# Optimization experiments

Measured on AMD Instinct MI355X. Metric: run time of the kernel, lower is better.

Reference implementation:

```python
import jax, jax.numpy as jnp
import numpy as np

N = 50000      # nodes
E = 400000     # edges
NODE_IN = 16
EDGE_IN = 8
H = 4          # heads (layer 1)
C = 64         # hidden_dim
HC = H * C     # 256


def setup_inputs() -> dict:
    key = jax.random.key(0)
    ks = iter(jax.random.split(key, 48))
    def rn(shape, s=0.05):
        return jax.random.normal(next(ks), shape, jnp.float32) * s
    x = jax.random.normal(next(ks), (N, NODE_IN), jnp.float32)
    edge_index = jax.random.randint(next(ks), (2, E), 0, N)
    edge_attr = jax.random.normal(next(ks), (E, EDGE_IN), jnp.float32)
    params = dict(
        # conv1: GATv2Conv(node_in -> hidden, heads=4, concat=True, edge_dim=edge_in)
        Wl1=rn((NODE_IN, HC)), bl1=jnp.zeros((HC,), jnp.float32),
        Wr1=rn((NODE_IN, HC)), br1=jnp.zeros((HC,), jnp.float32),
        We1=rn((EDGE_IN, HC)), att1=rn((H, C)), bias1=jnp.zeros((HC,), jnp.float32),
        # conv2: GATv2Conv(hidden*heads -> hidden, heads=1, concat=False)
        Wl2=rn((HC, C)), bl2=jnp.zeros((C,), jnp.float32),
        Wr2=rn((HC, C)), br2=jnp.zeros((C,), jnp.float32),
        We2=rn((EDGE_IN, C)), att2=rn((1, C)), bias2=jnp.zeros((C,), jnp.float32),
        # batchnorms (eval mode: running stats)
        bn1_g=jnp.ones((HC,), jnp.float32), bn1_b=jnp.zeros((HC,), jnp.float32),
        bn1_m=rn((HC,), 0.01), bn1_v=jnp.ones((HC,), jnp.float32),
        bn2_g=jnp.ones((C,), jnp.float32), bn2_b=jnp.zeros((C,), jnp.float32),
        bn2_m=rn((C,), 0.01), bn2_v=jnp.ones((C,), jnp.float32),
        # residual projection
        Wres=rn((NODE_IN, HC)),
        Wm1=rn((2 * C + EDGE_IN, C)), bm1=jnp.zeros((C,), jnp.float32),
        Wm2=rn((C, C // 2)), bm2=jnp.zeros((C // 2,), jnp.float32),
        Wm3=rn((C // 2, 1)), bm3=jnp.zeros((1,), jnp.float32),
    )
    return dict(x=x, edge_index=edge_index, edge_attr=edge_attr, **params)


def _gatv2(x, src, dst, e_attr, Wl, bl, Wr, br, We, att, bias, heads, out_ch, concat):
    """GATv2Conv message passing (PyG semantics, self-loops already in src/dst)."""
    n = x.shape[0]
    xl = (x @ Wl + bl).reshape(n, heads, out_ch)   # source transform
    xr = (x @ Wr + br).reshape(n, heads, out_ch)   # target transform
    ee = (e_attr @ We).reshape(-1, heads, out_ch)  # edge transform
    # per-edge attention logits: leaky_relu(x_i + x_j + e) . att
    m = jax.nn.leaky_relu(xl[src] + xr[dst] + ee, 0.2)        # [Etot, H, C]
    alpha = jnp.einsum('ehc,hc->eh', m, att)                  # [Etot, H]
    # segment softmax over destination nodes (every node has a self-loop)
    amax = jax.ops.segment_max(alpha, dst, num_segments=n)    # [N, H]
    expa = jnp.exp(alpha - amax[dst])
    denom = jax.ops.segment_sum(expa, dst, num_segments=n)    # [N, H]
    a = expa / (denom[dst] + 1e-16)
    out = jax.ops.segment_sum(xl[src] * a[:, :, None], dst, num_segments=n)  # [N, H, C]
    out = out.reshape(n, heads * out_ch) if concat else out.mean(axis=1)
    return out + bias


def _bn(h, g, b, m, v):
    return (h - m) * jax.lax.rsqrt(v + 1e-5) * g + b


def _forward(x, edge_attr, Wl1, bl1, Wr1, br1, We1, att1, bias1,
             Wl2, bl2, Wr2, br2, We2, att2, bias2,
             bn1_g, bn1_b, bn1_m, bn1_v, bn2_g, bn2_b, bn2_m, bn2_v,
             Wres, Wm1, bm1, Wm2, bm2, Wm3, bm3, edge_index):
    row, col = edge_index[0], edge_index[1]
    # add self-loops with fill_value='mean' for edge_attr (GATv2Conv default)
    loop = jnp.arange(N)
    src = jnp.concatenate([row, loop])
    dst = jnp.concatenate([col, loop])
    ea_mean = edge_attr.mean(axis=0, keepdims=True)
    ea_full = jnp.concatenate([edge_attr, jnp.broadcast_to(ea_mean, (N, EDGE_IN))], axis=0)
    h = _gatv2(x, src, dst, ea_full, Wl1, bl1, Wr1, br1, We1, att1, bias1, H, C, True)
    h = _bn(h, bn1_g, bn1_b, bn1_m, bn1_v)
    h = jax.nn.elu(h + x @ Wres)                 # residual; dropout is a no-op in eval
    h = _gatv2(h, src, dst, ea_full, Wl2, bl2, Wr2, br2, We2, att2, bias2, 1, C, False)
    h = _bn(h, bn2_g, bn2_b, bn2_m, bn2_v)
    h = jax.nn.elu(h)
    # edge head: gather endpoint embeddings + edge_attr -> MLP -> sigmoid
    er = jnp.concatenate([h[row], h[col], edge_attr], axis=-1)   # [E, 2C+edge_in]
    z = jax.nn.gelu(er @ Wm1 + bm1, approximate=False)
    z = jax.nn.gelu(z @ Wm2 + bm2, approximate=False)
    return jax.nn.sigmoid(z @ Wm3 + bm3)[:, 0]                    # [E]


def reference(x, edge_index, edge_attr, Wl1, bl1, Wr1, br1, We1, att1, bias1,
              Wl2, bl2, Wr2, br2, We2, att2, bias2,
              bn1_g, bn1_b, bn1_m, bn1_v, bn2_g, bn2_b, bn2_m, bn2_v,
              Wres, Wm1, bm1, Wm2, bm2, Wm3, bm3):
    return _forward(x, edge_attr, Wl1, bl1, Wr1, br1, We1, att1, bias1,
                    Wl2, bl2, Wr2, br2, We2, att2, bias2,
                    bn1_g, bn1_b, bn1_m, bn1_v, bn2_g, bn2_b, bn2_m, bn2_v,
                    Wres, Wm1, bm1, Wm2, bm2, Wm3, bm3, edge_index)
```

## Files before the change

kernel.cpp:

```cpp
#include <hip/hip_runtime.h>
#include <hip/hip_bf16.h>
#include <hip/hip_fp16.h>
#include <math.h>

#define NN 50000
#define EE 400000
#define ETOT (NN + EE)

__device__ __forceinline__ float gelu_f(float x) {
    return 0.5f * x * (1.f + erff(x * 0.7071067811865476f));
}
__device__ __forceinline__ float elu_f(float x) {
    return x > 0.f ? x : expm1f(x);
}
__device__ __forceinline__ float4 half8_lo_hi(uint4 raw, float4* hi) {
    __half2 h0 = *(__half2*)&raw.x, h1 = *(__half2*)&raw.y;
    __half2 h2 = *(__half2*)&raw.z, h3 = *(__half2*)&raw.w;
    float2 f0 = __half22float2(h0), f1 = __half22float2(h1);
    float2 f2 = __half22float2(h2), f3 = __half22float2(h3);
    *hi = make_float4(f2.x, f2.y, f3.x, f3.y);
    return make_float4(f0.x, f0.y, f1.x, f1.y);
}

__global__ __launch_bounds__(256) void k_ea_reduce(const float* __restrict__ ea,
                                                   float* __restrict__ ea_sum, int E) {
    float s[8];
#pragma unroll
    for (int i = 0; i < 8; i++) s[i] = 0.f;
    for (int e = blockIdx.x * blockDim.x + threadIdx.x; e < E; e += gridDim.x * blockDim.x) {
        const float4* p = (const float4*)(ea + (size_t)e * 8);
        float4 a = p[0], b = p[1];
        s[0] += a.x; s[1] += a.y; s[2] += a.z; s[3] += a.w;
        s[4] += b.x; s[5] += b.y; s[6] += b.z; s[7] += b.w;
    }
#pragma unroll
    for (int o = 32; o; o >>= 1)
#pragma unroll
        for (int i = 0; i < 8; i++) s[i] += __shfl_xor(s[i], o, 64);
    __shared__ float sh[4][8];
    int lane = threadIdx.x & 63, w = threadIdx.x >> 6;
    if (lane == 0)
#pragma unroll
        for (int i = 0; i < 8; i++) sh[w][i] = s[i];
    __syncthreads();
    if (threadIdx.x < 8) {
        float v = sh[0][threadIdx.x] + sh[1][threadIdx.x] + sh[2][threadIdx.x] + sh[3][threadIdx.x];
        atomicAdd(ea_sum + threadIdx.x, v);
    }
}

__global__ __launch_bounds__(256) void k_count(const int* __restrict__ ei, int* __restrict__ counts,
                                               int E, int N) {
    int e = blockIdx.x * blockDim.x + threadIdx.x;
    if (e >= E + N) return;
    int d = (e < E) ? ei[E + e] : (e - E);
    atomicAdd(counts + d, 1);
}

__global__ __launch_bounds__(1024) void k_scan(const int* __restrict__ counts, int* __restrict__ off,
                                               int* __restrict__ cursor, int N) {
    __shared__ int buf[1024];
    int t = threadIdx.x;
    int carry = 0;
    if (t == 0) off[0] = 0;
    for (int base = 0; base < N; base += 1024) {
        int i = base + t;
        int v = (i < N) ? counts[i] : 0;
        buf[t] = v;
        __syncthreads();
        for (int o = 1; o < 1024; o <<= 1) {
            int add = (t >= o) ? buf[t - o] : 0;
            __syncthreads();
            buf[t] += add;
            __syncthreads();
        }
        int incl = buf[t] + carry;
        if (i < N) { off[i + 1] = incl; cursor[i] = incl - v; }
        int tot = buf[1023];
        __syncthreads();
        carry += tot;
    }
}

__global__ __launch_bounds__(256) void k_scatter(const int* __restrict__ ei, int* __restrict__ cursor,
                                                 int* __restrict__ csr_src, int* __restrict__ csr_eid,
                                                 int E, int N) {
    int e = blockIdx.x * blockDim.x + threadIdx.x;
    if (e >= E + N) return;
    int s, d;
    if (e < E) { s = ei[e]; d = ei[E + e]; }
    else { s = d = e - E; }
    int pos = atomicAdd(cursor + d, 1);
    csr_src[pos] = s;
    csr_eid[pos] = e;
}

__global__ __launch_bounds__(256) void k_ntrans1(const float* __restrict__ x,
                                                 const float* __restrict__ Wl, const float* __restrict__ bl,
                                                 const float* __restrict__ Wr, const float* __restrict__ br,
                                                 __half* __restrict__ xl1h, float* __restrict__ xr1, int N) {
    __shared__ float swl[16 * 256];
    __shared__ float swr[16 * 256];
    __shared__ float sx[32 * 16];
    int t = threadIdx.x;
#pragma unroll
    for (int k = 0; k < 16; k++) { swl[k * 256 + t] = Wl[k * 256 + t]; swr[k * 256 + t] = Wr[k * 256 + t]; }
    int n0 = blockIdx.x * 32;
    for (int i = t; i < 32 * 16; i += 256) {
        int n = n0 + (i >> 4);
        sx[i] = (n < N) ? x[(size_t)n * 16 + (i & 15)] : 0.f;
    }
    __syncthreads();
    float bL = bl[t], bR = br[t];
    for (int ni = 0; ni < 32; ni++) {
        int n = n0 + ni;
        if (n >= N) break;
        float al = bL, ar = bR;
#pragma unroll
        for (int k = 0; k < 16; k++) {
            float xv = sx[ni * 16 + k];
            al += xv * swl[k * 256 + t];
            ar += xv * swr[k * 256 + t];
        }
        xl1h[(size_t)n * 256 + t] = __float2half(al);
        xr1[(size_t)n * 256 + t] = ar;
    }
}

__global__ __launch_bounds__(256) void k_fagg1(const __half* __restrict__ xl1h, const float* __restrict__ xr1,
                                               const int* __restrict__ off, const int* __restrict__ csr_src,
                                               const int* __restrict__ csr_eid,
                                               const float* __restrict__ ea, const float* __restrict__ ea_sum,
                                               const float* __restrict__ We1, const float* __restrict__ att1,
                                               const float* __restrict__ bias1,
                                               const float* __restrict__ x, const float* __restrict__ Wres,
                                               const float* __restrict__ g, const float* __restrict__ bb_,
                                               const float* __restrict__ mm_, const float* __restrict__ vv_,
                                               float* __restrict__ h1,
                                               int E, int N) {
    int t = threadIdx.x;
    int lane = t & 63, w = t >> 6;
    int node = blockIdx.x * 4 + w;
    if (node >= N) return;
    int c4 = lane * 4;
    float4 we[8];
#pragma unroll
    for (int k = 0; k < 8; k++) we[k] = *(const float4*)(We1 + k * 256 + c4);
    float4 xr4 = *(const float4*)(xr1 + (size_t)node * 256 + c4);
    float4 at4 = *(const float4*)(att1 + c4);
    float invE = 1.f / (float)E;
    float4 eam0, eam1;
    eam0.x = ea_sum[0] * invE; eam0.y = ea_sum[1] * invE;
    eam0.z = ea_sum[2] * invE; eam0.w = ea_sum[3] * invE;
    eam1.x = ea_sum[4] * invE; eam1.y = ea_sum[5] * invE;
    eam1.z = ea_sum[6] * invE; eam1.w = ea_sum[7] * invE;

    int beg = off[node], end = off[node + 1];
    float m = -1e30f, sumw = 0.f;
    float4 acc = make_float4(0.f, 0.f, 0.f, 0.f);

    int cb = beg;
    while (cb < end) {
        int cnt = end - cb; if (cnt > 64) cnt = 64;
        int sl = 0;
        float4 ba = eam0, bb4 = eam1;
        if (lane < cnt) {
            sl = csr_src[cb + lane];
            int el = csr_eid[cb + lane];
            if (el < E) {
                ba  = *(const float4*)(ea + (size_t)el * 8);
                bb4 = *(const float4*)(ea + (size_t)el * 8 + 4);
            }
        }
        float2 r0 = make_float2(0.f, 0.f), r1 = r0, r2 = r0;
        {
            int s0 = __shfl(sl, 0, 64);
            r0 = *(const float2*)(xl1h + (size_t)s0 * 256 + c4);
            if (cnt > 1) { int s1 = __shfl(sl, 1, 64); r1 = *(const float2*)(xl1h + (size_t)s1 * 256 + c4); }
            if (cnt > 2) { int s2 = __shfl(sl, 2, 64); r2 = *(const float2*)(xl1h + (size_t)s2 * 256 + c4); }
        }
        for (int j = 0; j < cnt; j++) {
            float2 cur = r0;
            r0 = r1; r1 = r2;
            if (j + 3 < cnt) {
                int s3 = __shfl(sl, j + 3, 64);
                r2 = *(const float2*)(xl1h + (size_t)s3 * 256 + c4);
            }
            float eav[8];
            eav[0] = __shfl(ba.x, j, 64);  eav[1] = __shfl(ba.y, j, 64);
            eav[2] = __shfl(ba.z, j, 64);  eav[3] = __shfl(ba.w, j, 64);
            eav[4] = __shfl(bb4.x, j, 64); eav[5] = __shfl(bb4.y, j, 64);
            eav[6] = __shfl(bb4.z, j, 64); eav[7] = __shfl(bb4.w, j, 64);
            const __half2* hp = (const __half2*)&cur;
            float2 lo = __half22float2(hp[0]);
            float2 hi = __half22float2(hp[1]);
            float4 xs = make_float4(lo.x, lo.y, hi.x, hi.y);
            float4 ee = make_float4(0.f, 0.f, 0.f, 0.f);
#pragma unroll
            for (int k = 0; k < 8; k++) {
                ee.x += eav[k] * we[k].x; ee.y += eav[k] * we[k].y;
                ee.z += eav[k] * we[k].z; ee.w += eav[k] * we[k].w;
            }
            float4 v;
            v.x = xs.x + xr4.x + ee.x; v.y = xs.y + xr4.y + ee.y;
            v.z = xs.z + xr4.z + ee.z; v.w = xs.w + xr4.w + ee.w;
            v.x = v.x > 0.f ? v.x : 0.2f * v.x;
            v.y = v.y > 0.f ? v.y : 0.2f * v.y;
            v.z = v.z > 0.f ? v.z : 0.2f * v.z;
            v.w = v.w > 0.f ? v.w : 0.2f * v.w;
            float p = v.x * at4.x + v.y * at4.y + v.z * at4.z + v.w * at4.w;
            p += __shfl_xor(p, 1, 64);
            p += __shfl_xor(p, 2, 64);
            p += __shfl_xor(p, 4, 64);
            p += __shfl_xor(p, 8, 64);
            float mn = fmaxf(m, p);
            float sc = expf(m - mn);
            float wgt = expf(p - mn);
            acc.x = acc.x * sc + wgt * xs.x;
            acc.y = acc.y * sc + wgt * xs.y;
            acc.z = acc.z * sc + wgt * xs.z;
            acc.w = acc.w * sc + wgt * xs.w;
            sumw = sumw * sc + wgt;
            m = mn;
        }
        cb += cnt;
    }
    float inv = 1.f / (sumw + 1e-16f);
    float4 r = make_float4(0.f, 0.f, 0.f, 0.f);
#pragma unroll
    for (int q = 0; q < 4; q++) {
        float4 xq = *(const float4*)(x + (size_t)node * 16 + q * 4);
        float xa[4] = { xq.x, xq.y, xq.z, xq.w };
#pragma unroll
        for (int kk = 0; kk < 4; kk++) {
            float4 wv = *(const float4*)(Wres + (size_t)(q * 4 + kk) * 256 + c4);
            r.x += xa[kk] * wv.x; r.y += xa[kk] * wv.y;
            r.z += xa[kk] * wv.z; r.w += xa[kk] * wv.w;
        }
    }
    float4 bi = *(const float4*)(bias1 + c4);
    float4 g4 = *(const float4*)(g + c4);
    float4 b4 = *(const float4*)(bb_ + c4);
    float4 m4 = *(const float4*)(mm_ + c4);
    float4 v4 = *(const float4*)(vv_ + c4);
    float4 o;
    o.x = acc.x * inv + bi.x; o.y = acc.y * inv + bi.y;
    o.z = acc.z * inv + bi.z; o.w = acc.w * inv + bi.w;
    o.x = (o.x - m4.x) * rsqrtf(v4.x + 1e-5f) * g4.x + b4.x + r.x;
    o.y = (o.y - m4.y) * rsqrtf(v4.y + 1e-5f) * g4.y + b4.y + r.y;
    o.z = (o.z - m4.z) * rsqrtf(v4.z + 1e-5f) * g4.z + b4.z + r.z;
    o.w = (o.w - m4.w) * rsqrtf(v4.w + 1e-5f) * g4.w + b4.w + r.w;
    o.x = elu_f(o.x); o.y = elu_f(o.y); o.z = elu_f(o.z); o.w = elu_f(o.w);
    *(float4*)(h1 + (size_t)node * 256 + c4) = o;
}

__global__ __launch_bounds__(256) void k_xlr2(const float* __restrict__ h1,
                                              const float* __restrict__ Wl2, const float* __restrict__ bl2,
                                              const float* __restrict__ Wr2, const float* __restrict__ br2,
                                              __half* __restrict__ xl2h, float* __restrict__ xr2, int N) {
    __shared__ float sh[32][32];
    __shared__ float sw[32][128];
    int t = threadIdx.x;
    int tr = t >> 5, tc = t & 31;
    int n0 = blockIdx.x * 32;
    float acc[4][4];
#pragma unroll
    for (int i = 0; i < 4; i++)
#pragma unroll
        for (int j = 0; j < 4; j++) acc[i][j] = 0.f;
    for (int k0 = 0; k0 < 256; k0 += 32) {
        {
            int n = t >> 3, kk0 = (t & 7) * 4;
            int gn = n0 + n;
            float4 hv = make_float4(0.f, 0.f, 0.f, 0.f);
            if (gn < N) hv = *(const float4*)(h1 + (size_t)gn * 256 + k0 + kk0);
            sh[kk0 + 0][n] = hv.x; sh[kk0 + 1][n] = hv.y; sh[kk0 + 2][n] = hv.z; sh[kk0 + 3][n] = hv.w;
        }
        for (int i = t; i < 32 * 128; i += 256) {
            int kk = i >> 7, c = i & 127;
            sw[kk][c] = (c < 64) ? Wl2[(size_t)(k0 + kk) * 64 + c] : Wr2[(size_t)(k0 + kk) * 64 + (c - 64)];
        }
        __syncthreads();
#pragma unroll
        for (int kk = 0; kk < 32; kk++) {
            float4 hv = *(const float4*)&sh[kk][tr * 4];
            float4 wv = *(const float4*)&sw[kk][tc * 4];
            float hh[4] = { hv.x, hv.y, hv.z, hv.w };
            float wwv[4] = { wv.x, wv.y, wv.z, wv.w };
#pragma unroll
            for (int i = 0; i < 4; i++)
#pragma unroll
                for (int j = 0; j < 4; j++) acc[i][j] += hh[i] * wwv[j];
        }
        __syncthreads();
    }
#pragma unroll
    for (int i = 0; i < 4; i++) {
        int gn = n0 + tr * 4 + i;
        if (gn >= N) continue;
#pragma unroll
        for (int j = 0; j < 4; j++) {
            int c = tc * 4 + j;
            float vv = acc[i][j];
            if (c < 64) xl2h[(size_t)gn * 64 + c] = __float2half(vv + bl2[c]);
            else        xr2[(size_t)gn * 64 + (c - 64)] = vv + br2[c - 64];
        }
    }
}

__global__ __launch_bounds__(256) void k_fagg2(const __half* __restrict__ xl2h, const float* __restrict__ xr2,
                                               const int* __restrict__ off, const int* __restrict__ csr_src,
                                               const int* __restrict__ csr_eid,
                                               const float* __restrict__ ea, const float* __restrict__ ea_sum,
                                               const float* __restrict__ We2, const float* __restrict__ att2,
                                               const float* __restrict__ bias2,
                                               const float* __restrict__ g, const float* __restrict__ bb_,
                                               const float* __restrict__ mm_, const float* __restrict__ vv_,
                                               __half* __restrict__ h2h,
                                               int E, int N) {
    int t = threadIdx.x;
    int lane = t & 63, w = t >> 6;
    int node = blockIdx.x * 4 + w;
    if (node >= N) return;
    float we[8];
#pragma unroll
    for (int k = 0; k < 8; k++) we[k] = We2[k * 64 + lane];
    float xr = xr2[(size_t)node * 64 + lane];
    float at = att2[lane];
    float invE = 1.f / (float)E;
    float4 eam0, eam1;
    eam0.x = ea_sum[0] * invE; eam0.y = ea_sum[1] * invE;
    eam0.z = ea_sum[2] * invE; eam0.w = ea_sum[3] * invE;
    eam1.x = ea_sum[4] * invE; eam1.y = ea_sum[5] * invE;
    eam1.z = ea_sum[6] * invE; eam1.w = ea_sum[7] * invE;

    int beg = off[node], end = off[node + 1];
    float m = -1e30f, sumw = 0.f, acc = 0.f;

    int cb = beg;
    while (cb < end) {
        int cnt = end - cb; if (cnt > 64) cnt = 64;
        int sl = 0;
        float4 ba = eam0, bb4 = eam1;
        if (lane < cnt) {
            sl = csr_src[cb + lane];
            int el = csr_eid[cb + lane];
            if (el < E) {
                ba  = *(const float4*)(ea + (size_t)el * 8);
                bb4 = *(const float4*)(ea + (size_t)el * 8 + 4);
            }
        }
        float r0 = 0.f, r1 = 0.f, r2 = 0.f;
        {
            int s0 = __shfl(sl, 0, 64);
            r0 = __half2float(xl2h[(size_t)s0 * 64 + lane]);
            if (cnt > 1) { int s1 = __shfl(sl, 1, 64); r1 = __half2float(xl2h[(size_t)s1 * 64 + lane]); }
            if (cnt > 2) { int s2 = __shfl(sl, 2, 64); r2 = __half2float(xl2h[(size_t)s2 * 64 + lane]); }
        }
        for (int j = 0; j < cnt; j++) {
            float xs = r0;
            r0 = r1; r1 = r2;
            if (j + 3 < cnt) {
                int s3 = __shfl(sl, j + 3, 64);
                r2 = __half2float(xl2h[(size_t)s3 * 64 + lane]);
            }
            float eav[8];
            eav[0] = __shfl(ba.x, j, 64);  eav[1] = __shfl(ba.y, j, 64);
            eav[2] = __shfl(ba.z, j, 64);  eav[3] = __shfl(ba.w, j, 64);
            eav[4] = __shfl(bb4.x, j, 64); eav[5] = __shfl(bb4.y, j, 64);
            eav[6] = __shfl(bb4.z, j, 64); eav[7] = __shfl(bb4.w, j, 64);
            float v = xs + xr;
#pragma unroll
            for (int k = 0; k < 8; k++) v += eav[k] * we[k];
            v = v > 0.f ? v : 0.2f * v;
            float p = v * at;
#pragma unroll
            for (int o = 32; o; o >>= 1) p += __shfl_xor(p, o, 64);
            float mn = fmaxf(m, p);
            float sc = expf(m - mn);
            float wgt = expf(p - mn);
            acc = acc * sc + wgt * xs;
            sumw = sumw * sc + wgt;
            m = mn;
        }
        cb += cnt;
    }
    float val = acc / (sumw + 1e-16f) + bias2[lane];
    val = (val - mm_[lane]) * rsqrtf(vv_[lane] + 1e-5f) * g[lane] + bb_[lane];
    h2h[(size_t)node * 64 + lane] = __float2half(elu_f(val));
}

__global__ __launch_bounds__(256) void k_uv(const __half* __restrict__ h2h, const float* __restrict__ Wm1,
                                            __half* __restrict__ uh, __half* __restrict__ vh, int N) {
    __shared__ float sh[32][32];
    __shared__ float sw[32][128];
    int t = threadIdx.x;
    int tr = t >> 5, tc = t & 31;
    int n0 = blockIdx.x * 32;
    float acc[4][4];
#pragma unroll
    for (int i = 0; i < 4; i++)
#pragma unroll
        for (int j = 0; j < 4; j++) acc[i][j] = 0.f;
    for (int k0 = 0; k0 < 64; k0 += 32) {
        {
            int n = t >> 3, kk0 = (t & 7) * 4;
            int gn = n0 + n;
            float4 hv = make_float4(0.f, 0.f, 0.f, 0.f);
            if (gn < N) {
                uint2 raw = *(const uint2*)(h2h + (size_t)gn * 64 + k0 + kk0);
                __half2 a = *(__half2*)&raw.x, b = *(__half2*)&raw.y;
                float2 fa = __half22float2(a), fb = __half22float2(b);
                hv = make_float4(fa.x, fa.y, fb.x, fb.y);
            }
            sh[kk0 + 0][n] = hv.x; sh[kk0 + 1][n] = hv.y; sh[kk0 + 2][n] = hv.z; sh[kk0 + 3][n] = hv.w;
        }
        for (int i = t; i < 32 * 128; i += 256) {
            int kk = i >> 7, c = i & 127;
            sw[kk][c] = (c < 64) ? Wm1[(size_t)(k0 + kk) * 64 + c]
                                 : Wm1[(size_t)(64 + k0 + kk) * 64 + (c - 64)];
        }
        __syncthreads();
#pragma unroll
        for (int kk = 0; kk < 32; kk++) {
            float4 hv = *(const float4*)&sh[kk][tr * 4];
            float4 wv = *(const float4*)&sw[kk][tc * 4];
            float hh[4] = { hv.x, hv.y, hv.z, hv.w };
            float wwv[4] = { wv.x, wv.y, wv.z, wv.w };
#pragma unroll
            for (int i = 0; i < 4; i++)
#pragma unroll
                for (int j = 0; j < 4; j++) acc[i][j] += hh[i] * wwv[j];
        }
        __syncthreads();
    }
#pragma unroll
    for (int i = 0; i < 4; i++) {
        int gn = n0 + tr * 4 + i;
        if (gn >= N) continue;
#pragma unroll
        for (int j = 0; j < 4; j++) {
            int c = tc * 4 + j;
            if (c < 64) uh[(size_t)gn * 64 + c] = __float2half(acc[i][j]);
            else        vh[(size_t)gn * 64 + (c - 64)] = __float2half(acc[i][j]);
        }
    }
}

__global__ __launch_bounds__(256) void k_wea(const float* __restrict__ ea, const float* __restrict__ Wm1,
                                             const float* __restrict__ bm1,
                                             __half* __restrict__ weAh, int E) {
    __shared__ float sW[8 * 64];
    int t = threadIdx.x;
    for (int i = t; i < 512; i += 256) sW[i] = Wm1[128 * 64 + i];
    __syncthreads();
    int i = blockIdx.x * 256 + t;
    if (i >= E * 8) return;
    int e = i >> 3, q = i & 7;
    float4 a0 = *(const float4*)(ea + (size_t)e * 8);
    float4 a1 = *(const float4*)(ea + (size_t)e * 8 + 4);
    float av[8] = { a0.x, a0.y, a0.z, a0.w, a1.x, a1.y, a1.z, a1.w };
    float o[8];
#pragma unroll
    for (int j = 0; j < 8; j++) o[j] = bm1[q * 8 + j];
#pragma unroll
    for (int k = 0; k < 8; k++) {
        float a = av[k];
#pragma unroll
        for (int j = 0; j < 8; j++) o[j] += a * sW[k * 64 + q * 8 + j];
    }
    __half2 h[4];
#pragma unroll
    for (int j = 0; j < 4; j++) h[j] = __floats2half2_rn(o[2 * j], o[2 * j + 1]);
    *(uint4*)(weAh + (size_t)e * 64 + q * 8) = *(uint4*)h;
}

__global__ __launch_bounds__(256) void k_mlp2(const __half* __restrict__ uh, const __half* __restrict__ vh,
                                              const __half* __restrict__ weAh, const int* __restrict__ ei,
                                              const float* __restrict__ Wm2, const float* __restrict__ bm2,
                                              const float* __restrict__ Wm3, const float* __restrict__ bm3,
                                              float* __restrict__ out, int E) {
    __shared__ float sw2[64 * 32];
    __shared__ int sre[64], sce[64];
    __shared__ float z1[64 * 68];
    int t = threadIdx.x;
    for (int i = t; i < 64 * 32; i += 256) sw2[i] = Wm2[i];
    int e0 = blockIdx.x * 64;
    if (t < 64) {
        int e = e0 + t;
        if (e < E) { sre[t] = ei[e]; sce[t] = ei[E + e]; }
        else { sre[t] = 0; sce[t] = 0; }
    }
    __syncthreads();
    for (int i = t; i < 512; i += 256) {
        int el = i >> 3, q = i & 7;
        int r = sre[el], c = sce[el];
        uint4 ru = *(const uint4*)(uh + (size_t)r * 64 + q * 8);
        uint4 rv = *(const uint4*)(vh + (size_t)c * 64 + q * 8);
        uint4 rw = *(const uint4*)(weAh + (size_t)(e0 + el) * 64 + q * 8);
        float4 uhi, vhi, whi;
        float4 ulo = half8_lo_hi(ru, &uhi);
        float4 vlo = half8_lo_hi(rv, &vhi);
        float4 wlo = half8_lo_hi(rw, &whi);
        float4 zlo, zhi;
        zlo.x = gelu_f(ulo.x + vlo.x + wlo.x);
        zlo.y = gelu_f(ulo.y + vlo.y + wlo.y);
        zlo.z = gelu_f(ulo.z + vlo.z + wlo.z);
        zlo.w = gelu_f(ulo.w + vlo.w + wlo.w);
        zhi.x = gelu_f(uhi.x + vhi.x + whi.x);
        zhi.y = gelu_f(uhi.y + vhi.y + whi.y);
        zhi.z = gelu_f(uhi.z + vhi.z + whi.z);
        zhi.w = gelu_f(uhi.w + vhi.w + whi.w);
        *(float4*)(z1 + el * 68 + q * 8)     = zlo;
        *(float4*)(z1 + el * 68 + q * 8 + 4) = zhi;
    }
    __syncthreads();
    int tr = t >> 3;
    int tc = t & 7;
    float b2[4], w3[4];
#pragma unroll
    for (int j = 0; j < 4; j++) { b2[j] = bm2[tc * 4 + j]; w3[j] = Wm3[tc * 4 + j]; }
    float b3 = bm3[0];
    float acc0[4], acc1[4];
#pragma unroll
    for (int j = 0; j < 4; j++) { acc0[j] = 0.f; acc1[j] = 0.f; }
    const float* z0p = z1 + (tr * 2 + 0) * 68;
    const float* z1p = z1 + (tr * 2 + 1) * 68;
#pragma unroll 8
    for (int k = 0; k < 64; k++) {
        float4 wv = *(const float4*)(sw2 + k * 32 + tc * 4);
        float a0 = z0p[k];
        float a1 = z1p[k];
        acc0[0] += a0 * wv.x; acc0[1] += a0 * wv.y; acc0[2] += a0 * wv.z; acc0[3] += a0 * wv.w;
        acc1[0] += a1 * wv.x; acc1[1] += a1 * wv.y; acc1[2] += a1 * wv.z; acc1[3] += a1 * wv.w;
    }
    float p0 = 0.f, p1 = 0.f;
#pragma unroll
    for (int j = 0; j < 4; j++) {
        p0 += gelu_f(acc0[j] + b2[j]) * w3[j];
        p1 += gelu_f(acc1[j] + b2[j]) * w3[j];
    }
    p0 += __shfl_xor(p0, 1, 64); p0 += __shfl_xor(p0, 2, 64); p0 += __shfl_xor(p0, 4, 64);
    p1 += __shfl_xor(p1, 1, 64); p1 += __shfl_xor(p1, 2, 64); p1 += __shfl_xor(p1, 4, 64);
    if (tc == 0) {
        int e = e0 + tr * 2;
        if (e < E)     out[e]     = 1.f / (1.f + expf(-(p0 + b3)));
        if (e + 1 < E) out[e + 1] = 1.f / (1.f + expf(-(p1 + b3)));
    }
}

extern "C" void kernel_launch(void* const* d_in, const int* in_sizes, int n_in,
                              void* d_out, int out_size, void* d_ws, size_t ws_size,
                              hipStream_t stream) {
    const float* x    = (const float*)d_in[0];
    const int*   ei   = (const int*)d_in[1];
    const float* ea   = (const float*)d_in[2];
    const float* Wl1  = (const float*)d_in[3];
    const float* bl1  = (const float*)d_in[4];
    const float* Wr1  = (const float*)d_in[5];
    const float* br1  = (const float*)d_in[6];
    const float* We1  = (const float*)d_in[7];
    const float* att1 = (const float*)d_in[8];
    const float* bias1= (const float*)d_in[9];
    const float* Wl2  = (const float*)d_in[10];
    const float* bl2  = (const float*)d_in[11];
    const float* Wr2  = (const float*)d_in[12];
    const float* br2  = (const float*)d_in[13];
    const float* We2  = (const float*)d_in[14];
    const float* att2 = (const float*)d_in[15];
    const float* bias2= (const float*)d_in[16];
    const float* bn1g = (const float*)d_in[17];
    const float* bn1b = (const float*)d_in[18];
    const float* bn1m = (const float*)d_in[19];
    const float* bn1v = (const float*)d_in[20];
    const float* bn2g = (const float*)d_in[21];
    const float* bn2b = (const float*)d_in[22];
    const float* bn2m = (const float*)d_in[23];
    const float* bn2v = (const float*)d_in[24];
    const float* Wres = (const float*)d_in[25];
    const float* Wm1  = (const float*)d_in[26];
    const float* bm1  = (const float*)d_in[27];
    const float* Wm2  = (const float*)d_in[28];
    const float* bm2  = (const float*)d_in[29];
    const float* Wm3  = (const float*)d_in[30];
    const float* bm3  = (const float*)d_in[31];
    float* out = (float*)d_out;
    float* ws = (float*)d_ws;

    const int N = NN, E = EE, Etot = ETOT;

    float* ea_sum   = ws;
    int*   counts   = (int*)(ws + 16);
    int*   off      = (int*)(ws + 16 + (size_t)N);
    int*   cursor   = (int*)(ws + 32 + (size_t)2 * N);
    int*   csr_src  = (int*)(ws + 32 + (size_t)3 * N);
    int*   csr_eid  = (int*)(ws + 32 + (size_t)3 * N + Etot);
    size_t base     = 32 + (size_t)3 * N + (size_t)2 * Etot;
    __half* xl1h    = (__half*)(ws + base);
    __half* xl2h    = xl1h;
    __half* h2h     = (__half*)(ws + base + (size_t)128 * N);
    float* xr1      = ws + base + (size_t)160 * N;
    float* h1       = xr1;
    __half* weAh    = (__half*)xr1;
    float* xr2      = xr1 + (size_t)256 * N;
    __half* uh      = (__half*)xr2;
    __half* vh      = uh + (size_t)64 * N;

    hipMemsetAsync(ea_sum, 0, 16 * sizeof(float), stream);
    hipMemsetAsync(counts, 0, (size_t)N * sizeof(int), stream);

    k_ea_reduce<<<256, 256, 0, stream>>>(ea, ea_sum, E);
    k_count<<<(Etot + 255) / 256, 256, 0, stream>>>(ei, counts, E, N);
    k_scan<<<1, 1024, 0, stream>>>(counts, off, cursor, N);
    k_scatter<<<(Etot + 255) / 256, 256, 0, stream>>>(ei, cursor, csr_src, csr_eid, E, N);
    k_ntrans1<<<(N + 31) / 32, 256, 0, stream>>>(x, Wl1, bl1, Wr1, br1, xl1h, xr1, N);
    k_fagg1<<<(N + 3) / 4, 256, 0, stream>>>(xl1h, xr1, off, csr_src, csr_eid, ea, ea_sum,
                                             We1, att1, bias1, x, Wres,
                                             bn1g, bn1b, bn1m, bn1v, h1, E, N);
    k_xlr2<<<(N + 31) / 32, 256, 0, stream>>>(h1, Wl2, bl2, Wr2, br2, xl2h, xr2, N);
    k_fagg2<<<(N + 3) / 4, 256, 0, stream>>>(xl2h, xr2, off, csr_src, csr_eid, ea, ea_sum,
                                             We2, att2, bias2,
                                             bn2g, bn2b, bn2m, bn2v, h2h, E, N);
    k_wea<<<(E * 8 + 255) / 256, 256, 0, stream>>>(ea, Wm1, bm1, weAh, E);
    k_uv<<<(N + 31) / 32, 256, 0, stream>>>(h2h, Wm1, uh, vh, N);
    k_mlp2<<<(E + 63) / 64, 256, 0, stream>>>(uh, vh, weAh, ei, Wm2, bm2, Wm3, bm3, out, E);
}
```

Before: 549.9 us.

## Process edges in pairs in GAT aggregation, prefetch edge attrs per edge, vectorize scan

Both GATv2 aggregation kernels now handle two edges per iteration, folding their two logits into the online softmax with one rescale, and prefetch the next pair's source rows. Edge attributes are loaded as uniform broadcast float4 loads per edge instead of per-lane loads followed by eight shuffles per edge. The CSR offset scan now has each thread handle four counts, so there are fewer block-wide scan passes. The aim is to cut shuffle traffic, exp count and loop latency, at the cost of more registers and redundant broadcast loads across lanes.

```diff
diff --git a/kernel.cpp b/kernel.cpp
--- a/kernel.cpp
+++ b/kernel.cpp
@@ -63,10 +63,20 @@
     int t = threadIdx.x;
     int carry = 0;
     if (t == 0) off[0] = 0;
-    for (int base = 0; base < N; base += 1024) {
-        int i = base + t;
-        int v = (i < N) ? counts[i] : 0;
-        buf[t] = v;
+    for (int base = 0; base < N; base += 4096) {
+        int i0 = base + t * 4;
+        int v0 = 0, v1 = 0, v2 = 0, v3 = 0;
+        if (i0 + 3 < N) {
+            int4 vv = *(const int4*)(counts + i0);
+            v0 = vv.x; v1 = vv.y; v2 = vv.z; v3 = vv.w;
+        } else {
+            if (i0 < N)     v0 = counts[i0];
+            if (i0 + 1 < N) v1 = counts[i0 + 1];
+            if (i0 + 2 < N) v2 = counts[i0 + 2];
+            if (i0 + 3 < N) v3 = counts[i0 + 3];
+        }
+        int s01 = v0 + v1, s012 = s01 + v2, tot4 = s012 + v3;
+        buf[t] = tot4;
         __syncthreads();
         for (int o = 1; o < 1024; o <<= 1) {
             int add = (t >= o) ? buf[t - o] : 0;
@@ -74,8 +84,12 @@
             buf[t] += add;
             __syncthreads();
         }
-        int incl = buf[t] + carry;
-        if (i < N) { off[i + 1] = incl; cursor[i] = incl - v; }
+        int incl4 = buf[t] + carry;
+        int excl = incl4 - tot4;
+        if (i0 < N)     { off[i0 + 1] = excl + v0;   cursor[i0]     = excl; }
+        if (i0 + 1 < N) { off[i0 + 2] = excl + s01;  cursor[i0 + 1] = excl + v0; }
+        if (i0 + 2 < N) { off[i0 + 3] = excl + s012; cursor[i0 + 2] = excl + s01; }
+        if (i0 + 3 < N) { off[i0 + 4] = excl + tot4; cursor[i0 + 3] = excl + s012; }
         int tot = buf[1023];
         __syncthreads();
         carry += tot;
@@ -127,6 +141,53 @@
     }
 }
 
+__device__ __forceinline__ void fetch1_c1(const __half* __restrict__ xl1h, const float* __restrict__ ea,
+                                          int sl, int el, int j, int cnt, int c4,
+                                          float4 eam0, float4 eam1, int E,
+                                          float2* row, float4* e0, float4* e1) {
+    if (j < cnt) {
+        int s = __shfl(sl, j, 64);
+        int e = __shfl(el, j, 64);
+        *row = *(const float2*)(xl1h + (size_t)s * 256 + c4);
+        if (e < E) {
+            *e0 = *(const float4*)(ea + (size_t)e * 8);
+            *e1 = *(const float4*)(ea + (size_t)e * 8 + 4);
+        } else { *e0 = eam0; *e1 = eam1; }
+    } else {
+        *row = make_float2(0.f, 0.f); *e0 = eam0; *e1 = eam1;
+    }
+}
+
+__device__ __forceinline__ float logit_c1(float2 raw, float4 e0, float4 e1,
+                                          const float4* we, float4 xr4, float4 at4,
+                                          float4* xs_out) {
+    const __half2* hp = (const __half2*)&raw;
+    float2 lo = __half22float2(hp[0]);
+    float2 hi = __half22float2(hp[1]);
+    float4 xs = make_float4(lo.x, lo.y, hi.x, hi.y);
+    float ev[8] = { e0.x, e0.y, e0.z, e0.w, e1.x, e1.y, e1.z, e1.w };
+    float4 ee = make_float4(0.f, 0.f, 0.f, 0.f);
+#pragma unroll
+    for (int k = 0; k < 8; k++) {
+        ee.x += ev[k] * we[k].x; ee.y += ev[k] * we[k].y;
+        ee.z += ev[k] * we[k].z; ee.w += ev[k] * we[k].w;
+    }
+    float4 v;
+    v.x = xs.x + xr4.x + ee.x; v.y = xs.y + xr4.y + ee.y;
+    v.z = xs.z + xr4.z + ee.z; v.w = xs.w + xr4.w + ee.w;
+    v.x = v.x > 0.f ? v.x : 0.2f * v.x;
+    v.y = v.y > 0.f ? v.y : 0.2f * v.y;
+    v.z = v.z > 0.f ? v.z : 0.2f * v.z;
+    v.w = v.w > 0.f ? v.w : 0.2f * v.w;
+    float p = v.x * at4.x + v.y * at4.y + v.z * at4.z + v.w * at4.w;
+    p += __shfl_xor(p, 1, 64);
+    p += __shfl_xor(p, 2, 64);
+    p += __shfl_xor(p, 4, 64);
+    p += __shfl_xor(p, 8, 64);
+    *xs_out = xs;
+    return p;
+}
+
 __global__ __launch_bounds__(256) void k_fagg1(const __half* __restrict__ xl1h, const float* __restrict__ xr1,
                                                const int* __restrict__ off, const int* __restrict__ csr_src,
                                                const int* __restrict__ csr_eid,
@@ -162,66 +223,42 @@
     int cb = beg;
     while (cb < end) {
         int cnt = end - cb; if (cnt > 64) cnt = 64;
-        int sl = 0;
-        float4 ba = eam0, bb4 = eam1;
-        if (lane < cnt) {
-            sl = csr_src[cb + lane];
-            int el = csr_eid[cb + lane];
-            if (el < E) {
-                ba  = *(const float4*)(ea + (size_t)el * 8);
-                bb4 = *(const float4*)(ea + (size_t)el * 8 + 4);
+        int sl = 0, el = 0;
+        if (lane < cnt) { sl = csr_src[cb + lane]; el = csr_eid[cb + lane]; }
+        float2 rA, rB, rC, rD;
+        float4 a0, a1, b0, b1, c0, c1, d0, d1;
+        fetch1_c1(xl1h, ea, sl, el, 0, cnt, c4, eam0, eam1, E, &rA, &a0, &a1);
+        fetch1_c1(xl1h, ea, sl, el, 1, cnt, c4, eam0, eam1, E, &rB, &b0, &b1);
+        for (int j = 0; j < cnt; j += 2) {
+            fetch1_c1(xl1h, ea, sl, el, j + 2, cnt, c4, eam0, eam1, E, &rC, &c0, &c1);
+            fetch1_c1(xl1h, ea, sl, el, j + 3, cnt, c4, eam0, eam1, E, &rD, &d0, &d1);
+            float4 xsA, xsB;
+            float pA = logit_c1(rA, a0, a1, we, xr4, at4, &xsA);
+            if (j + 1 < cnt) {
+                float pB = logit_c1(rB, b0, b1, we, xr4, at4, &xsB);
+                float mn = fmaxf(m, fmaxf(pA, pB));
+                float sc = expf(m - mn);
+                float wa = expf(pA - mn);
+                float wb = expf(pB - mn);
+                acc.x = acc.x * sc + wa * xsA.x + wb * xsB.x;
+                acc.y = acc.y * sc + wa * xsA.y + wb * xsB.y;
+                acc.z = acc.z * sc + wa * xsA.z + wb * xsB.z;
+                acc.w = acc.w * sc + wa * xsA.w + wb * xsB.w;
+                sumw = sumw * sc + wa + wb;
+                m = mn;
+            } else {
+                float mn = fmaxf(m, pA);
+                float sc = expf(m - mn);
+                float wa = expf(pA - mn);
+                acc.x = acc.x * sc + wa * xsA.x;
+                acc.y = acc.y * sc + wa * xsA.y;
+                acc.z = acc.z * sc + wa * xsA.z;
+                acc.w = acc.w * sc + wa * xsA.w;
+                sumw = sumw * sc + wa;
+                m = mn;
             }
-        }
-        float2 r0 = make_float2(0.f, 0.f), r1 = r0, r2 = r0;
-        {
-            int s0 = __shfl(sl, 0, 64);
-            r0 = *(const float2*)(xl1h + (size_t)s0 * 256 + c4);
-            if (cnt > 1) { int s1 = __shfl(sl, 1, 64); r1 = *(const float2*)(xl1h + (size_t)s1 * 256 + c4); }
-            if (cnt > 2) { int s2 = __shfl(sl, 2, 64); r2 = *(const float2*)(xl1h + (size_t)s2 * 256 + c4); }
-        }
-        for (int j = 0; j < cnt; j++) {
-            float2 cur = r0;
-            r0 = r1; r1 = r2;
-            if (j + 3 < cnt) {
-                int s3 = __shfl(sl, j + 3, 64);
-                r2 = *(const float2*)(xl1h + (size_t)s3 * 256 + c4);
-            }
-            float eav[8];
-            eav[0] = __shfl(ba.x, j, 64);  eav[1] = __shfl(ba.y, j, 64);
-            eav[2] = __shfl(ba.z, j, 64);  eav[3] = __shfl(ba.w, j, 64);
-            eav[4] = __shfl(bb4.x, j, 64); eav[5] = __shfl(bb4.y, j, 64);
-            eav[6] = __shfl(bb4.z, j, 64); eav[7] = __shfl(bb4.w, j, 64);
-            const __half2* hp = (const __half2*)&cur;
-            float2 lo = __half22float2(hp[0]);
-            float2 hi = __half22float2(hp[1]);
-            float4 xs = make_float4(lo.x, lo.y, hi.x, hi.y);
-            float4 ee = make_float4(0.f, 0.f, 0.f, 0.f);
-#pragma unroll
-            for (int k = 0; k < 8; k++) {
-                ee.x += eav[k] * we[k].x; ee.y += eav[k] * we[k].y;
-                ee.z += eav[k] * we[k].z; ee.w += eav[k] * we[k].w;
-            }
-            float4 v;
-            v.x = xs.x + xr4.x + ee.x; v.y = xs.y + xr4.y + ee.y;
-            v.z = xs.z + xr4.z + ee.z; v.w = xs.w + xr4.w + ee.w;
-            v.x = v.x > 0.f ? v.x : 0.2f * v.x;
-            v.y = v.y > 0.f ? v.y : 0.2f * v.y;
-            v.z = v.z > 0.f ? v.z : 0.2f * v.z;
-            v.w = v.w > 0.f ? v.w : 0.2f * v.w;
-            float p = v.x * at4.x + v.y * at4.y + v.z * at4.z + v.w * at4.w;
-            p += __shfl_xor(p, 1, 64);
-            p += __shfl_xor(p, 2, 64);
-            p += __shfl_xor(p, 4, 64);
-            p += __shfl_xor(p, 8, 64);
-            float mn = fmaxf(m, p);
-            float sc = expf(m - mn);
-            float wgt = expf(p - mn);
-            acc.x = acc.x * sc + wgt * xs.x;
-            acc.y = acc.y * sc + wgt * xs.y;
-            acc.z = acc.z * sc + wgt * xs.z;
-            acc.w = acc.w * sc + wgt * xs.w;
-            sumw = sumw * sc + wgt;
-            m = mn;
+            rA = rC; a0 = c0; a1 = c1;
+            rB = rD; b0 = d0; b1 = d1;
         }
         cb += cnt;
     }
@@ -308,6 +345,36 @@
     }
 }
 
+__device__ __forceinline__ void fetch1_c2(const __half* __restrict__ xl2h, const float* __restrict__ ea,
+                                          int sl, int el, int j, int cnt, int lane,
+                                          float4 eam0, float4 eam1, int E,
+                                          float* row, float4* e0, float4* e1) {
+    if (j < cnt) {
+        int s = __shfl(sl, j, 64);
+        int e = __shfl(el, j, 64);
+        *row = __half2float(xl2h[(size_t)s * 64 + lane]);
+        if (e < E) {
+            *e0 = *(const float4*)(ea + (size_t)e * 8);
+            *e1 = *(const float4*)(ea + (size_t)e * 8 + 4);
+        } else { *e0 = eam0; *e1 = eam1; }
+    } else {
+        *row = 0.f; *e0 = eam0; *e1 = eam1;
+    }
+}
+
+__device__ __forceinline__ float logit_c2(float xs, float4 e0, float4 e1,
+                                          const float* we, float xr, float at) {
+    float ev[8] = { e0.x, e0.y, e0.z, e0.w, e1.x, e1.y, e1.z, e1.w };
+    float v = xs + xr;
+#pragma unroll
+    for (int k = 0; k < 8; k++) v += ev[k] * we[k];
+    v = v > 0.f ? v : 0.2f * v;
+    float p = v * at;
+#pragma unroll
+    for (int o = 32; o; o >>= 1) p += __shfl_xor(p, o, 64);
+    return p;
+}
+
 __global__ __launch_bounds__(256) void k_fagg2(const __half* __restrict__ xl2h, const float* __restrict__ xr2,
                                                const int* __restrict__ off, const int* __restrict__ csr_src,
                                                const int* __restrict__ csr_eid,
@@ -340,48 +407,35 @@
     int cb = beg;
     while (cb < end) {
         int cnt = end - cb; if (cnt > 64) cnt = 64;
-        int sl = 0;
-        float4 ba = eam0, bb4 = eam1;
-        if (lane < cnt) {
-            sl = csr_src[cb + lane];
-            int el = csr_eid[cb + lane];
-            if (el < E) {
-                ba  = *(const float4*)(ea + (size_t)el * 8);
-                bb4 = *(const float4*)(ea + (size_t)el * 8 + 4);
+        int sl = 0, el = 0;
+        if (lane < cnt) { sl = csr_src[cb + lane]; el = csr_eid[cb + lane]; }
+        float rA, rB, rC, rD;
+        float4 a0, a1, b0, b1, c0, c1, d0, d1;
+        fetch1_c2(xl2h, ea, sl, el, 0, cnt, lane, eam0, eam1, E, &rA, &a0, &a1);
+        fetch1_c2(xl2h, ea, sl, el, 1, cnt, lane, eam0, eam1, E, &rB, &b0, &b1);
+        for (int j = 0; j < cnt; j += 2) {
+            fetch1_c2(xl2h, ea, sl, el, j + 2, cnt, lane, eam0, eam1, E, &rC, &c0, &c1);
+            fetch1_c2(xl2h, ea, sl, el, j + 3, cnt, lane, eam0, eam1, E, &rD, &d0, &d1);
+            float pA = logit_c2(rA, a0, a1, we, xr, at);
+            if (j + 1 < cnt) {
+                float pB = logit_c2(rB, b0, b1, we, xr, at);
+                float mn = fmaxf(m, fmaxf(pA, pB));
+                float sc = expf(m - mn);
+                float wa = expf(pA - mn);
+                float wb = expf(pB - mn);
+                acc = acc * sc + wa * rA + wb * rB;
+                sumw = sumw * sc + wa + wb;
+                m = mn;
+            } else {
+                float mn = fmaxf(m, pA);
+                float sc = expf(m - mn);
+                float wa = expf(pA - mn);
+                acc = acc * sc + wa * rA;
+                sumw = sumw * sc + wa;
+                m = mn;
             }
-        }
-        float r0 = 0.f, r1 = 0.f, r2 = 0.f;
-        {
-            int s0 = __shfl(sl, 0, 64);
-            r0 = __half2float(xl2h[(size_t)s0 * 64 + lane]);
-            if (cnt > 1) { int s1 = __shfl(sl, 1, 64); r1 = __half2float(xl2h[(size_t)s1 * 64 + lane]); }
-            if (cnt > 2) { int s2 = __shfl(sl, 2, 64); r2 = __half2float(xl2h[(size_t)s2 * 64 + lane]); }
-        }
-        for (int j = 0; j < cnt; j++) {
-            float xs = r0;
-            r0 = r1; r1 = r2;
-            if (j + 3 < cnt) {
-                int s3 = __shfl(sl, j + 3, 64);
-                r2 = __half2float(xl2h[(size_t)s3 * 64 + lane]);
-            }
-            float eav[8];
-            eav[0] = __shfl(ba.x, j, 64);  eav[1] = __shfl(ba.y, j, 64);
-            eav[2] = __shfl(ba.z, j, 64);  eav[3] = __shfl(ba.w, j, 64);
-            eav[4] = __shfl(bb4.x, j, 64); eav[5] = __shfl(bb4.y, j, 64);
-            eav[6] = __shfl(bb4.z, j, 64); eav[7] = __shfl(bb4.w, j, 64);
-            float v = xs + xr;
-#pragma unroll
-            for (int k = 0; k < 8; k++) v += eav[k] * we[k];
-            v = v > 0.f ? v : 0.2f * v;
-            float p = v * at;
-#pragma unroll
-            for (int o = 32; o; o >>= 1) p += __shfl_xor(p, o, 64);
-            float mn = fmaxf(m, p);
-            float sc = expf(m - mn);
-            float wgt = expf(p - mn);
-            acc = acc * sc + wgt * xs;
-            sumw = sumw * sc + wgt;
-            m = mn;
+            rA = rC; a0 = c0; a1 = c1;
+            rB = rD; b0 = d0; b1 = d1;
         }
         cb += cnt;
     }
```

Result: slower. 595.4 us (+8.3%).

## Fuse preprocessing kernels and compute edge-attr MLP term inside final MLP

Applied to the files above, without the earlier changes.

Merges the edge-attr reduction and degree count into one launch, and the CSR scatter and first node transform into one launch by partitioning blocks. Drops the separate weA kernel, so the final MLP kernel now computes the edge-attr contribution from raw edge features instead of writing and reading a half-precision E×64 intermediate. The scan now handles four elements per thread to cut loop iterations. The cost is some extra arithmetic per edge in the MLP kernel and extra shared memory that may lower occupancy.

```diff
diff --git a/kernel.cpp b/kernel.cpp
--- a/kernel.cpp
+++ b/kernel.cpp
@@ -22,39 +22,40 @@
     return make_float4(f0.x, f0.y, f1.x, f1.y);
 }
 
-__global__ __launch_bounds__(256) void k_ea_reduce(const float* __restrict__ ea,
-                                                   float* __restrict__ ea_sum, int E) {
-    float s[8];
-#pragma unroll
-    for (int i = 0; i < 8; i++) s[i] = 0.f;
-    for (int e = blockIdx.x * blockDim.x + threadIdx.x; e < E; e += gridDim.x * blockDim.x) {
-        const float4* p = (const float4*)(ea + (size_t)e * 8);
-        float4 a = p[0], b = p[1];
-        s[0] += a.x; s[1] += a.y; s[2] += a.z; s[3] += a.w;
-        s[4] += b.x; s[5] += b.y; s[6] += b.z; s[7] += b.w;
-    }
-#pragma unroll
-    for (int o = 32; o; o >>= 1)
-#pragma unroll
-        for (int i = 0; i < 8; i++) s[i] += __shfl_xor(s[i], o, 64);
-    __shared__ float sh[4][8];
-    int lane = threadIdx.x & 63, w = threadIdx.x >> 6;
-    if (lane == 0)
-#pragma unroll
-        for (int i = 0; i < 8; i++) sh[w][i] = s[i];
-    __syncthreads();
-    if (threadIdx.x < 8) {
-        float v = sh[0][threadIdx.x] + sh[1][threadIdx.x] + sh[2][threadIdx.x] + sh[3][threadIdx.x];
-        atomicAdd(ea_sum + threadIdx.x, v);
-    }
-}
-
-__global__ __launch_bounds__(256) void k_count(const int* __restrict__ ei, int* __restrict__ counts,
-                                               int E, int N) {
-    int e = blockIdx.x * blockDim.x + threadIdx.x;
-    if (e >= E + N) return;
-    int d = (e < E) ? ei[E + e] : (e - E);
-    atomicAdd(counts + d, 1);
+__global__ __launch_bounds__(256) void k_init(const float* __restrict__ ea, float* __restrict__ ea_sum,
+                                              const int* __restrict__ ei, int* __restrict__ counts,
+                                              int E, int N) {
+    int t = threadIdx.x;
+    if (blockIdx.x < 256) {
+        float s[8];
+#pragma unroll
+        for (int i = 0; i < 8; i++) s[i] = 0.f;
+        for (int e = blockIdx.x * 256 + t; e < E; e += 256 * 256) {
+            const float4* p = (const float4*)(ea + (size_t)e * 8);
+            float4 a = p[0], b = p[1];
+            s[0] += a.x; s[1] += a.y; s[2] += a.z; s[3] += a.w;
+            s[4] += b.x; s[5] += b.y; s[6] += b.z; s[7] += b.w;
+        }
+#pragma unroll
+        for (int o = 32; o; o >>= 1)
+#pragma unroll
+            for (int i = 0; i < 8; i++) s[i] += __shfl_xor(s[i], o, 64);
+        __shared__ float sh[4][8];
+        int lane = t & 63, w = t >> 6;
+        if (lane == 0)
+#pragma unroll
+            for (int i = 0; i < 8; i++) sh[w][i] = s[i];
+        __syncthreads();
+        if (t < 8) {
+            float v = sh[0][t] + sh[1][t] + sh[2][t] + sh[3][t];
+            atomicAdd(ea_sum + t, v);
+        }
+    } else {
+        int e = (blockIdx.x - 256) * 256 + t;
+        if (e >= E + N) return;
+        int d = (e < E) ? ei[E + e] : (e - E);
+        atomicAdd(counts + d, 1);
+    }
 }
 
 __global__ __launch_bounds__(1024) void k_scan(const int* __restrict__ counts, int* __restrict__ off,
@@ -63,10 +64,20 @@
     int t = threadIdx.x;
     int carry = 0;
     if (t == 0) off[0] = 0;
-    for (int base = 0; base < N; base += 1024) {
-        int i = base + t;
-        int v = (i < N) ? counts[i] : 0;
-        buf[t] = v;
+    for (int base = 0; base < N; base += 4096) {
+        int i0 = base + t * 4;
+        int v0 = 0, v1 = 0, v2 = 0, v3 = 0;
+        if (i0 + 3 < N) {
+            int4 vv = *(const int4*)(counts + i0);
+            v0 = vv.x; v1 = vv.y; v2 = vv.z; v3 = vv.w;
+        } else {
+            if (i0 < N)     v0 = counts[i0];
+            if (i0 + 1 < N) v1 = counts[i0 + 1];
+            if (i0 + 2 < N) v2 = counts[i0 + 2];
+            if (i0 + 3 < N) v3 = counts[i0 + 3];
+        }
+        int s01 = v0 + v1, s012 = s01 + v2, tot4 = s012 + v3;
+        buf[t] = tot4;
         __syncthreads();
         for (int o = 1; o < 1024; o <<= 1) {
             int add = (t >= o) ? buf[t - o] : 0;
@@ -74,38 +85,45 @@
             buf[t] += add;
             __syncthreads();
         }
-        int incl = buf[t] + carry;
-        if (i < N) { off[i + 1] = incl; cursor[i] = incl - v; }
+        int incl4 = buf[t] + carry;
+        int excl = incl4 - tot4;
+        if (i0 < N)     { off[i0 + 1] = excl + v0;   cursor[i0]     = excl; }
+        if (i0 + 1 < N) { off[i0 + 2] = excl + s01;  cursor[i0 + 1] = excl + v0; }
+        if (i0 + 2 < N) { off[i0 + 3] = excl + s012; cursor[i0 + 2] = excl + s01; }
+        if (i0 + 3 < N) { off[i0 + 4] = excl + tot4; cursor[i0 + 3] = excl + s012; }
         int tot = buf[1023];
         __syncthreads();
         carry += tot;
     }
 }
 
-__global__ __launch_bounds__(256) void k_scatter(const int* __restrict__ ei, int* __restrict__ cursor,
-                                                 int* __restrict__ csr_src, int* __restrict__ csr_eid,
-                                                 int E, int N) {
-    int e = blockIdx.x * blockDim.x + threadIdx.x;
-    if (e >= E + N) return;
-    int s, d;
-    if (e < E) { s = ei[e]; d = ei[E + e]; }
-    else { s = d = e - E; }
-    int pos = atomicAdd(cursor + d, 1);
-    csr_src[pos] = s;
-    csr_eid[pos] = e;
-}
-
-__global__ __launch_bounds__(256) void k_ntrans1(const float* __restrict__ x,
-                                                 const float* __restrict__ Wl, const float* __restrict__ bl,
-                                                 const float* __restrict__ Wr, const float* __restrict__ br,
-                                                 __half* __restrict__ xl1h, float* __restrict__ xr1, int N) {
+__global__ __launch_bounds__(256) void k_scat_nt1(const int* __restrict__ ei, int* __restrict__ cursor,
+                                                  int* __restrict__ csr_src, int* __restrict__ csr_eid,
+                                                  const float* __restrict__ x,
+                                                  const float* __restrict__ Wl, const float* __restrict__ bl,
+                                                  const float* __restrict__ Wr, const float* __restrict__ br,
+                                                  __half* __restrict__ xl1h, float* __restrict__ xr1,
+                                                  int E, int N) {
     __shared__ float swl[16 * 256];
     __shared__ float swr[16 * 256];
     __shared__ float sx[32 * 16];
     int t = threadIdx.x;
+    int S = (E + N + 255) >> 8;
+    if ((int)blockIdx.x < S) {
+        int e = blockIdx.x * 256 + t;
+        if (e >= E + N) return;
+        int s, d;
+        if (e < E) { s = ei[e]; d = ei[E + e]; }
+        else { s = d = e - E; }
+        int pos = atomicAdd(cursor + d, 1);
+        csr_src[pos] = s;
+        csr_eid[pos] = e;
+        return;
+    }
+    int bid = blockIdx.x - S;
 #pragma unroll
     for (int k = 0; k < 16; k++) { swl[k * 256 + t] = Wl[k * 256 + t]; swr[k * 256 + t] = Wr[k * 256 + t]; }
-    int n0 = blockIdx.x * 32;
+    int n0 = bid * 32;
     for (int i = t; i < 32 * 16; i += 256) {
         int n = n0 + (i >> 4);
         sx[i] = (n < N) ? x[(size_t)n * 16 + (i & 15)] : 0.f;
@@ -447,44 +465,21 @@
     }
 }
 
-__global__ __launch_bounds__(256) void k_wea(const float* __restrict__ ea, const float* __restrict__ Wm1,
-                                             const float* __restrict__ bm1,
-                                             __half* __restrict__ weAh, int E) {
-    __shared__ float sW[8 * 64];
-    int t = threadIdx.x;
-    for (int i = t; i < 512; i += 256) sW[i] = Wm1[128 * 64 + i];
-    __syncthreads();
-    int i = blockIdx.x * 256 + t;
-    if (i >= E * 8) return;
-    int e = i >> 3, q = i & 7;
-    float4 a0 = *(const float4*)(ea + (size_t)e * 8);
-    float4 a1 = *(const float4*)(ea + (size_t)e * 8 + 4);
-    float av[8] = { a0.x, a0.y, a0.z, a0.w, a1.x, a1.y, a1.z, a1.w };
-    float o[8];
-#pragma unroll
-    for (int j = 0; j < 8; j++) o[j] = bm1[q * 8 + j];
-#pragma unroll
-    for (int k = 0; k < 8; k++) {
-        float a = av[k];
-#pragma unroll
-        for (int j = 0; j < 8; j++) o[j] += a * sW[k * 64 + q * 8 + j];
-    }
-    __half2 h[4];
-#pragma unroll
-    for (int j = 0; j < 4; j++) h[j] = __floats2half2_rn(o[2 * j], o[2 * j + 1]);
-    *(uint4*)(weAh + (size_t)e * 64 + q * 8) = *(uint4*)h;
-}
-
 __global__ __launch_bounds__(256) void k_mlp2(const __half* __restrict__ uh, const __half* __restrict__ vh,
-                                              const __half* __restrict__ weAh, const int* __restrict__ ei,
+                                              const float* __restrict__ ea, const int* __restrict__ ei,
+                                              const float* __restrict__ Wm1, const float* __restrict__ bm1,
                                               const float* __restrict__ Wm2, const float* __restrict__ bm2,
                                               const float* __restrict__ Wm3, const float* __restrict__ bm3,
                                               float* __restrict__ out, int E) {
     __shared__ float sw2[64 * 32];
+    __shared__ float sW1e[8 * 64];
+    __shared__ float sb1[64];
     __shared__ int sre[64], sce[64];
     __shared__ float z1[64 * 68];
     int t = threadIdx.x;
     for (int i = t; i < 64 * 32; i += 256) sw2[i] = Wm2[i];
+    for (int i = t; i < 512; i += 256) sW1e[i] = Wm1[128 * 64 + i];
+    if (t < 64) sb1[t] = bm1[t];
     int e0 = blockIdx.x * 64;
     if (t < 64) {
         int e = e0 + t;
@@ -497,20 +492,30 @@
         int r = sre[el], c = sce[el];
         uint4 ru = *(const uint4*)(uh + (size_t)r * 64 + q * 8);
         uint4 rv = *(const uint4*)(vh + (size_t)c * 64 + q * 8);
-        uint4 rw = *(const uint4*)(weAh + (size_t)(e0 + el) * 64 + q * 8);
-        float4 uhi, vhi, whi;
+        float4 a0 = *(const float4*)(ea + (size_t)(e0 + el) * 8);
+        float4 a1 = *(const float4*)(ea + (size_t)(e0 + el) * 8 + 4);
+        float av[8] = { a0.x, a0.y, a0.z, a0.w, a1.x, a1.y, a1.z, a1.w };
+        float wv[8];
+#pragma unroll
+        for (int j = 0; j < 8; j++) wv[j] = sb1[q * 8 + j];
+#pragma unroll
+        for (int k = 0; k < 8; k++) {
+            float a = av[k];
+#pragma unroll
+            for (int j = 0; j < 8; j++) wv[j] += a * sW1e[k * 64 + q * 8 + j];
+        }
+        float4 uhi, vhi;
         float4 ulo = half8_lo_hi(ru, &uhi);
         float4 vlo = half8_lo_hi(rv, &vhi);
-        float4 wlo = half8_lo_hi(rw, &whi);
         float4 zlo, zhi;
-        zlo.x = gelu_f(ulo.x + vlo.x + wlo.x);
-        zlo.y = gelu_f(ulo.y + vlo.y + wlo.y);
-        zlo.z = gelu_f(ulo.z + vlo.z + wlo.z);
-        zlo.w = gelu_f(ulo.w + vlo.w + wlo.w);
-        zhi.x = gelu_f(uhi.x + vhi.x + whi.x);
-        zhi.y = gelu_f(uhi.y + vhi.y + whi.y);
-        zhi.z = gelu_f(uhi.z + vhi.z + whi.z);
-        zhi.w = gelu_f(uhi.w + vhi.w + whi.w);
+        zlo.x = gelu_f(ulo.x + vlo.x + wv[0]);
+        zlo.y = gelu_f(ulo.y + vlo.y + wv[1]);
+        zlo.z = gelu_f(ulo.z + vlo.z + wv[2]);
+        zlo.w = gelu_f(ulo.w + vlo.w + wv[3]);
+        zhi.x = gelu_f(uhi.x + vhi.x + wv[4]);
+        zhi.y = gelu_f(uhi.y + vhi.y + wv[5]);
+        zhi.z = gelu_f(uhi.z + vhi.z + wv[6]);
+        zhi.w = gelu_f(uhi.w + vhi.w + wv[7]);
         *(float4*)(z1 + el * 68 + q * 8)     = zlo;
         *(float4*)(z1 + el * 68 + q * 8 + 4) = zhi;
     }
@@ -601,7 +606,6 @@
     __half* h2h     = (__half*)(ws + base + (size_t)128 * N);
     float* xr1      = ws + base + (size_t)160 * N;
     float* h1       = xr1;
-    __half* weAh    = (__half*)xr1;
     float* xr2      = xr1 + (size_t)256 * N;
     __half* uh      = (__half*)xr2;
     __half* vh      = uh + (size_t)64 * N;
@@ -609,11 +613,11 @@
     hipMemsetAsync(ea_sum, 0, 16 * sizeof(float), stream);
     hipMemsetAsync(counts, 0, (size_t)N * sizeof(int), stream);
 
-    k_ea_reduce<<<256, 256, 0, stream>>>(ea, ea_sum, E);
-    k_count<<<(Etot + 255) / 256, 256, 0, stream>>>(ei, counts, E, N);
+    int S = (Etot + 255) / 256;
+    k_init<<<256 + S, 256, 0, stream>>>(ea, ea_sum, ei, counts, E, N);
     k_scan<<<1, 1024, 0, stream>>>(counts, off, cursor, N);
-    k_scatter<<<(Etot + 255) / 256, 256, 0, stream>>>(ei, cursor, csr_src, csr_eid, E, N);
-    k_ntrans1<<<(N + 31) / 32, 256, 0, stream>>>(x, Wl1, bl1, Wr1, br1, xl1h, xr1, N);
+    k_scat_nt1<<<S + (N + 31) / 32, 256, 0, stream>>>(ei, cursor, csr_src, csr_eid,
+                                                      x, Wl1, bl1, Wr1, br1, xl1h, xr1, E, N);
     k_fagg1<<<(N + 3) / 4, 256, 0, stream>>>(xl1h, xr1, off, csr_src, csr_eid, ea, ea_sum,
                                              We1, att1, bias1, x, Wres,
                                              bn1g, bn1b, bn1m, bn1v, h1, E, N);
@@ -621,7 +625,6 @@
     k_fagg2<<<(N + 3) / 4, 256, 0, stream>>>(xl2h, xr2, off, csr_src, csr_eid, ea, ea_sum,
                                              We2, att2, bias2,
                                              bn2g, bn2b, bn2m, bn2v, h2h, E, N);
-    k_wea<<<(E * 8 + 255) / 256, 256, 0, stream>>>(ea, Wm1, bm1, weAh, E);
     k_uv<<<(N + 31) / 32, 256, 0, stream>>>(h2h, Wm1, uh, vh, N);
-    k_mlp2<<<(E + 63) / 64, 256, 0, stream>>>(uh, vh, weAh, ei, Wm2, bm2, Wm3, bm3, out, E);
-}
+    k_mlp2<<<(E + 63) / 64, 256, 0, stream>>>(uh, vh, ea, ei, Wm1, bm1, Wm2, bm2, Wm3, bm3, out, E);
+}
```

Measured after the change: 506.1 us. -8.0%, faster.
